# Kernel optimization log

Hardware: AMD Instinct MI355X
Metric: run time of the kernel (lower is better)

## Reference

```python
import jax, jax.numpy as jnp
import numpy as np

N, D_IM, D_CLI = 2048, 1024, 64
EPS = 1e-12  # F.normalize eps


def setup_inputs() -> dict:
    key = jax.random.key(0)
    k1, k2, k3, k4 = jax.random.split(key, 4)
    phi_im = jax.random.normal(k1, (N, D_IM), dtype=jnp.float32)
    phi_cli = jax.random.normal(k2, (N, D_CLI), dtype=jnp.float32)
    t = jax.random.randint(k3, (N, 2), 0, 3, dtype=jnp.int64)
    traumatic = jax.random.randint(k4, (N,), 0, 2, dtype=jnp.int64)
    return {"phi_im": phi_im, "phi_cli": phi_cli, "t": t, "traumatic": traumatic}


def _l2norm(x):
    n = jnp.sqrt(jnp.sum(x * x, axis=1, keepdims=True))
    return x / jnp.maximum(n, EPS)


def _pair_block(S, ma, mb):
    # S: [N,N] full cosine similarity; ma, mb: [N] bool group masks.
    valid = ma[:, None] & mb[None, :]
    mat = jnp.where(valid, S, 0.0)            # scatter-into-zero matrix semantics
    masked = jnp.where(valid, S, jnp.inf)     # masked argmin = nearest (least similar) pair
    flat = jnp.argmin(masked.reshape(-1))
    i = flat // S.shape[1]
    j = flat % S.shape[1]
    return mat, masked.reshape(-1)[flat], jnp.stack([i, j])


def reference(phi_im, phi_cli, t, traumatic):
    im_n = _l2norm(phi_im)
    cli_n = _l2norm(phi_cli)
    # single batched GEMM replaces the per-pair python loops
    S_im = im_n @ im_n.T    # [N,N]
    S_cli = cli_n @ cli_n.T  # [N,N]

    t1 = t[:, 1]
    m0 = (t1 == 0) & (traumatic == 1)
    m1 = t1 == 1
    m2 = t1 == 2

    mats, vals, idxs = [], [], []
    for S in (S_im, S_cli):
        for (ma, mb) in ((m0, m1), (m0, m2), (m1, m2)):
            mat, v, ij = _pair_block(S, ma, mb)
            mats.append(mat)
            vals.append(v)
            idxs.append(ij)
    sims = jnp.stack(mats)           # [6, N, N]: im_01, im_02, im_12, cli_01, cli_02, cli_12
    min_vals = jnp.stack(vals)       # [6]
    min_idx = jnp.stack(idxs)        # [6, 2]
    return sims, min_vals, min_idx
```

## Files before the change

### kernel.cpp

```cpp
#include <hip/hip_runtime.h>
#include <stdint.h>

#define NROW 2048
#define D_IM 1024
#define D_CLI 64
#define EPSF 1e-12f
#define NN ((size_t)NROW * (size_t)NROW)
#define GRID_GEMM 800
#define PIM_STRIDE 4352

typedef __attribute__((ext_vector_type(8))) short bf16x8;
typedef __attribute__((ext_vector_type(4))) float f32x4;

#define OFF_PACKED   0
#define OFF_CNT      64
#define OFF_CAT      128
#define OFF_LISTS    8320
#define OFF_POS      32896
#define OFF_COLINFO  41216
#define OFF_INVIM    65792
#define OFF_INVCLI   73984
#define OFF_PIM      82176
#define OFF_PCLI     8995072
#define OFF_SC       9519360

__device__ __forceinline__ unsigned int enc_f32(float x) {
    unsigned int u = __float_as_uint(x);
    return (u & 0x80000000u) ? ~u : (u | 0x80000000u);
}
__device__ __forceinline__ unsigned short bf16rn(float x) {
    unsigned int u = __float_as_uint(x);
    return (unsigned short)((u + 0x7FFFu + ((u >> 16) & 1u)) >> 16);
}
__device__ __forceinline__ float bf16tof(unsigned short h) {
    return __uint_as_float(((unsigned int)h) << 16);
}

__global__ __launch_bounds__(256)
void prepscan_kernel(const float* __restrict__ phi_im,
                     const float* __restrict__ phi_cli,
                     const int* __restrict__ t,
                     const int* __restrict__ traumatic,
                     float* __restrict__ inv_im,
                     float* __restrict__ inv_cli,
                     char* __restrict__ pim,
                     char* __restrict__ pcli,
                     int* __restrict__ cnt,
                     int* __restrict__ catArr,
                     int* __restrict__ lists,
                     int* __restrict__ posIn,
                     unsigned int* __restrict__ colinfo,
                     unsigned long long* __restrict__ packed,
                     float* __restrict__ out) {
    __shared__ unsigned long long shmem[256];
    const int tid = threadIdx.x;

    if (blockIdx.x > NROW) {
        const int row = blockIdx.x - (NROW + 1);
        const int t1 = t[2 * row + 1];
        const int tr = traumatic[row];
        if (t1 == 0 && tr == 1) return;
        float* orow = out + (size_t)row * NROW;
        const f32x4 z4 = (f32x4){0.f, 0.f, 0.f, 0.f};
        __builtin_nontemporal_store(z4, (f32x4*)orow + tid);
        __builtin_nontemporal_store(z4, (f32x4*)orow + tid + 256);
        return;
    }

    if (blockIdx.x == NROW) {
        int cats[8];
        unsigned long long mycnt = 0;
        #pragma unroll
        for (int e = 0; e < 8; e++) {
            int r = tid * 8 + e;
            int t1 = t[2 * r + 1];
            int tr = traumatic[r];
            int c = (t1 == 1) ? 1 : ((t1 == 2) ? 2 : ((tr == 1) ? 0 : 3));
            cats[e] = c;
            catArr[r] = c;
            if (c < 3) mycnt += 1ULL << (21 * c);
        }
        shmem[tid] = mycnt;
        __syncthreads();
        for (int off = 1; off < 256; off <<= 1) {
            unsigned long long v = (tid >= off) ? shmem[tid - off] : 0ULL;
            __syncthreads();
            shmem[tid] += v;
            __syncthreads();
        }
        unsigned long long excl = shmem[tid] - mycnt;
        unsigned long long tot = shmem[255];
        unsigned int loc[3];
        #pragma unroll
        for (int c = 0; c < 3; c++)
            loc[c] = (unsigned int)(excl >> (21 * c)) & 0x1FFFFFu;
        #pragma unroll
        for (int e = 0; e < 8; e++) {
            int r = tid * 8 + e;
            int c = cats[e];
            unsigned int slot = 0xFFFFFFFFu;
            if (c < 3) {
                slot = loc[c]++;
                lists[c * 2048 + slot] = r;
                posIn[r] = (int)slot;
            }
            colinfo[0 * 2048 + r] = (c == 1) ? slot : 0xFFFFFFFFu;
            colinfo[1 * 2048 + r] = (c == 2) ? slot : 0xFFFFFFFFu;
            colinfo[2 * 2048 + r] = (c == 2) ? slot : 0xFFFFFFFFu;
        }
        if (tid == 0) {
            cnt[0] = (int)(tot & 0x1FFFFFu);
            cnt[1] = (int)((tot >> 21) & 0x1FFFFFu);
            cnt[2] = (int)((tot >> 42) & 0x1FFFFFu);
            cnt[3] = 0;
        }
        if (tid < 6) packed[tid] = 0xFFFFFFFFFFFFFFFFULL;
        return;
    }

    float* sred = (float*)shmem;
    const int r = blockIdx.x;

    float4 v = ((const float4*)(phi_im + (size_t)r * D_IM))[tid];
    float a[4] = {v.x, v.y, v.z, v.w};
    unsigned short h4[4], l4[4];
    #pragma unroll
    for (int e = 0; e < 4; e++) {
        h4[e] = bf16rn(a[e]);
        l4[e] = bf16rn(a[e] - bf16tof(h4[e]));
    }
    {
        char* rowb = pim + (size_t)r * PIM_STRIDE + (tid >> 1) * 32 + (tid & 1) * 8;
        *(ushort4*)rowb = make_ushort4(h4[0], h4[1], h4[2], h4[3]);
        *(ushort4*)(rowb + 16) = make_ushort4(l4[0], l4[1], l4[2], l4[3]);
    }
    sred[tid] = a[0] * a[0] + a[1] * a[1] + a[2] * a[2] + a[3] * a[3];
    __syncthreads();
    for (int off = 128; off > 0; off >>= 1) {
        if (tid < off) sred[tid] += sred[tid + off];
        __syncthreads();
    }
    if (tid == 0) inv_im[r] = 1.0f / fmaxf(sqrtf(sred[0]), EPSF);

    if (tid < 16) {
        float4 c = ((const float4*)(phi_cli + (size_t)r * D_CLI))[tid];
        float b[4] = {c.x, c.y, c.z, c.w};
        unsigned short ch[4], cl[4];
        #pragma unroll
        for (int e = 0; e < 4; e++) {
            ch[e] = bf16rn(b[e]);
            cl[e] = bf16rn(b[e] - bf16tof(ch[e]));
        }
        char* rowb = pcli + (size_t)r * 256 + (tid >> 1) * 32 + (tid & 1) * 8;
        *(ushort4*)rowb = make_ushort4(ch[0], ch[1], ch[2], ch[3]);
        *(ushort4*)(rowb + 16) = make_ushort4(cl[0], cl[1], cl[2], cl[3]);
    }
    if (tid < 64) {
        float c = phi_cli[(size_t)r * D_CLI + tid];
        float cs = c * c;
        #pragma unroll
        for (int off = 32; off > 0; off >>= 1) cs += __shfl_down(cs, off, 64);
        if (tid == 0) inv_cli[r] = 1.0f / fmaxf(sqrtf(cs), EPSF);
    }
}

#define MFMA_SET(AH, AL, BH, BL)                                           \
    _Pragma("unroll") for (int lm = 0; lm < 2; lm++)                       \
        _Pragma("unroll") for (int ln = 0; ln < 2; ln++) {                 \
            acc[lm][ln] = __builtin_amdgcn_mfma_f32_16x16x32_bf16(         \
                AH[lm], BH[ln], acc[lm][ln], 0, 0, 0);                     \
            acc[lm][ln] = __builtin_amdgcn_mfma_f32_16x16x32_bf16(         \
                AH[lm], BL[ln], acc[lm][ln], 0, 0, 0);                     \
            acc[lm][ln] = __builtin_amdgcn_mfma_f32_16x16x32_bf16(         \
                AL[lm], BH[ln], acc[lm][ln], 0, 0, 0);                     \
        }

#define LOAD_REGS(RA, RB, OFF)                                             \
    RA[0] = *(const f32x4*)(pX + gA0 + (OFF));                             \
    RA[1] = *(const f32x4*)(pX + gA1 + (OFF));                             \
    RB[0] = *(const f32x4*)(pX + gB0 + (OFF));                             \
    RB[1] = *(const f32x4*)(pX + gB1 + (OFF));

#define STAGE_WRITE(B, RA, RB)                                             \
    *(f32x4*)(&sT[B][0][my_e][my_r * 16]) = RA[0];                         \
    *(f32x4*)(&sT[B][0][my_e][(32 + my_r) * 16]) = RA[1];                  \
    *(f32x4*)(&sT[B][1][my_e][my_r * 16]) = RB[0];                         \
    *(f32x4*)(&sT[B][1][my_e][(32 + my_r) * 16]) = RB[1];

#define COMPUTE(B)                                                         \
    {                                                                      \
        bf16x8 AH[2], AL[2], BH[2], BL[2];                                 \
        _Pragma("unroll") for (int q = 0; q < 2; q++) {                    \
            AH[q] = *(const bf16x8*)(&sT[B][0][2 * quad][aoff[q]]);        \
            AL[q] = *(const bf16x8*)(&sT[B][0][2 * quad + 1][aoff[q]]);    \
            BH[q] = *(const bf16x8*)(&sT[B][1][2 * quad][boff[q]]);        \
            BL[q] = *(const bf16x8*)(&sT[B][1][2 * quad + 1][boff[q]]);    \
        }                                                                  \
        MFMA_SET(AH, AL, BH, BL)                                           \
    }

__global__ __launch_bounds__(256, 2)
void gemm_kernel(const char* __restrict__ pim,
                 const char* __restrict__ pcli,
                 const float* __restrict__ inv_im,
                 const float* __restrict__ inv_cli,
                 const int* __restrict__ cnt,
                 const int* __restrict__ lists,
                 const int* __restrict__ catArr,
                 unsigned short* __restrict__ Sc,
                 float* __restrict__ out,
                 unsigned long long* __restrict__ packed) {
    const int tid = threadIdx.x;

    if (blockIdx.x >= GRID_GEMM) {
        const int b = blockIdx.x - GRID_GEMM;
        const int pzf = 1 + (b >> 11);
        const int row = b & 2047;
        const int p = (pzf < 3) ? pzf : pzf - 3;
        const int rowcat = (p == 2) ? 1 : 0;
        if (catArr[row] == rowcat) return;
        float* orow = out + (size_t)pzf * NN + (size_t)row * NROW;
        const f32x4 z4 = (f32x4){0.f, 0.f, 0.f, 0.f};
        __builtin_nontemporal_store(z4, (f32x4*)orow + tid);
        __builtin_nontemporal_store(z4, (f32x4*)orow + tid + 256);
        return;
    }

    __shared__ float sIA[64], sIB[64];
    __shared__ int sRA[64], sRB[64];
    __shared__ __align__(16) char sT[2][2][8][1040];

    const int n0 = cnt[0], n1 = cnt[1], n2 = cnt[2];
    const int tA = (n0 + 63) >> 6, tB = (n1 + 63) >> 6, tC = (n2 + 63) >> 6;
    const int T0 = tA * tB, T1 = tA * tC, T2 = tB * tC;
    const int tot = T0 + T1 + T2;
    int bid = blockIdx.x;
    if (bid >= 2 * tot) return;
    int z = 0;
    if (bid >= tot) { z = 1; bid -= tot; }
    const size_t s0 = (size_t)(tA << 6) * (tB << 6);
    const size_t s1 = (size_t)(tA << 6) * (tC << 6);
    const size_t s2 = (size_t)(tB << 6) * (tC << 6);
    size_t scoff = z ? (s0 + s1 + s2) : 0;
    int gx, nA, nB, nBpad, pp;
    const int *lA, *lB;
    if (bid < T0)           { pp = 0; gx = tB; nA = n0; nB = n1; lA = lists;        lB = lists + 2048; nBpad = tB << 6; }
    else if (bid < T0 + T1) { bid -= T0;      scoff += s0;      pp = 1; gx = tC; nA = n0; nB = n2; lA = lists;        lB = lists + 4096; nBpad = tC << 6; }
    else                    { bid -= T0 + T1; scoff += s0 + s1; pp = 2; gx = tC; nA = n1; nB = n2; lA = lists + 2048; lB = lists + 4096; nBpad = tC << 6; }
    const int by = bid / gx, bx = bid % gx;
    const int i0 = by << 6, j0 = bx << 6;
    const int pz = z * 3 + pp;

    const char* __restrict__ pX = z ? pcli : pim;
    const float* __restrict__ inv = z ? inv_cli : inv_im;
    const int nst = z ? (D_CLI / 32) : (D_IM / 32);
    const size_t stride = z ? 256 : PIM_STRIDE;
    const int lane = tid & 63;
    const int wid = tid >> 6;
    const int wr = wid >> 1;
    const int wc = wid & 1;

    if (tid < 64) {
        int ia = lA[min(i0 + tid, nA - 1)];
        int ib = lB[min(j0 + tid, nB - 1)];
        sRA[tid] = ia; sRB[tid] = ib;
        sIA[tid] = inv[ia]; sIB[tid] = inv[ib];
    }
    __syncthreads();

    const int mrow = lane & 15;
    const int quad = lane >> 4;

    const int my_e = tid & 7;
    const int my_r = tid >> 3;
    const size_t gA0 = (size_t)sRA[my_r] * stride + my_e * 16;
    const size_t gA1 = (size_t)sRA[32 + my_r] * stride + my_e * 16;
    const size_t gB0 = (size_t)sRB[my_r] * stride + my_e * 16;
    const size_t gB1 = (size_t)sRB[32 + my_r] * stride + my_e * 16;

    int aoff[2], boff[2];
    #pragma unroll
    for (int q = 0; q < 2; q++) {
        aoff[q] = ((wr * 2 + q) * 16 + mrow) * 16;
        boff[q] = ((wc * 2 + q) * 16 + mrow) * 16;
    }

    f32x4 acc[2][2];
    #pragma unroll
    for (int lm = 0; lm < 2; lm++)
        #pragma unroll
        for (int ln = 0; ln < 2; ln++)
            acc[lm][ln] = (f32x4){0.f, 0.f, 0.f, 0.f};

    f32x4 ra0[2], rb0[2], ra1[2], rb1[2];
    LOAD_REGS(ra0, rb0, 0);
    LOAD_REGS(ra1, rb1, 128);

    for (int st = 0; st < nst; st += 2) {
        STAGE_WRITE(0, ra0, rb0);
        __syncthreads();
        if (st + 2 < nst) { LOAD_REGS(ra0, rb0, (size_t)(st + 2) * 128); }
        COMPUTE(0);
        __syncthreads();

        STAGE_WRITE(1, ra1, rb1);
        __syncthreads();
        if (st + 3 < nst) { LOAD_REGS(ra1, rb1, (size_t)(st + 3) * 128); }
        COMPUTE(1);
        __syncthreads();
    }

    unsigned long long best = 0xFFFFFFFFFFFFFFFFULL;
    #pragma unroll
    for (int lm = 0; lm < 2; lm++)
        #pragma unroll
        for (int ln = 0; ln < 2; ln++) {
            const int cloc = (wc * 2 + ln) * 16 + mrow;
            const float ivb = sIB[cloc];
            const unsigned int jcol = (unsigned int)sRB[cloc];
            #pragma unroll
            for (int rr = 0; rr < 4; rr++) {
                const int rloc = (wr * 2 + lm) * 16 + quad * 4 + rr;
                float sv = acc[lm][ln][rr] * (sIA[rloc] * ivb);
                Sc[scoff + (size_t)(i0 + rloc) * nBpad + (j0 + cloc)] = bf16rn(sv);
                unsigned long long pk =
                    ((unsigned long long)enc_f32(sv) << 32) |
                    ((unsigned int)sRA[rloc] * (unsigned int)NROW + jcol);
                if (pk < best) best = pk;
            }
        }
    #pragma unroll
    for (int off = 32; off > 0; off >>= 1) {
        unsigned long long o = __shfl_down(best, off, 64);
        if (o < best) best = o;
    }
    if (lane == 0) atomicMin(&packed[pz], best);
}

__global__ __launch_bounds__(256)
void writer_kernel(const unsigned short* __restrict__ Sc,
                   const int* __restrict__ cnt,
                   const int* __restrict__ catArr,
                   const int* __restrict__ posIn,
                   const unsigned int* __restrict__ colinfo,
                   float* __restrict__ out,
                   const unsigned long long* __restrict__ packed) {
    const int b = blockIdx.x;
    const int tid = threadIdx.x;
    if (b == 6 * NROW) {
        const int p = tid;
        if (p < 6) {
            unsigned long long pk = packed[p];
            float v;
            unsigned int flat;
            if (pk == 0xFFFFFFFFFFFFFFFFULL) { v = __builtin_huge_valf(); flat = 0u; }
            else {
                unsigned int key = (unsigned int)(pk >> 32);
                flat = (unsigned int)pk;
                unsigned int bits = (key & 0x80000000u) ? (key ^ 0x80000000u) : ~key;
                v = __uint_as_float(bits);
            }
            out[6 * NN + p] = v;
            out[6 * NN + 6 + 2 * p + 0] = (float)(flat >> 11);
            out[6 * NN + 6 + 2 * p + 1] = (float)(flat & 2047u);
        }
        return;
    }
    const int pz = b >> 11;
    const int row = b & 2047;
    const int z = pz / 3, p = pz - 3 * z;

    const int rowcat = (p == 2) ? 1 : 0;
    if (catArr[row] != rowcat) {
        if (pz < 4) return;
        float* orow = out + (size_t)pz * NN + (size_t)row * NROW;
        const f32x4 z4 = (f32x4){0.f, 0.f, 0.f, 0.f};
        __builtin_nontemporal_store(z4, (f32x4*)orow + tid);
        __builtin_nontemporal_store(z4, (f32x4*)orow + tid + 256);
        return;
    }

    float* orow = out + (size_t)pz * NN + (size_t)row * NROW;

    const int n0 = cnt[0], n1 = cnt[1], n2 = cnt[2];
    const int tA = (n0 + 63) >> 6, tB = (n1 + 63) >> 6, tC = (n2 + 63) >> 6;
    const size_t s0 = (size_t)(tA << 6) * (tB << 6);
    const size_t s1 = (size_t)(tA << 6) * (tC << 6);
    const size_t s2 = (size_t)(tB << 6) * (tC << 6);
    size_t scoff = z ? (s0 + s1 + s2) : 0;
    int nBpad;
    if (p == 0)      { nBpad = tB << 6; }
    else if (p == 1) { scoff += s0;      nBpad = tC << 6; }
    else             { scoff += s0 + s1; nBpad = tC << 6; }

    const unsigned short* srow = Sc + scoff + (size_t)posIn[row] * nBpad;
    const uint4* cinfo4 = (const uint4*)(colinfo + p * 2048);

    #pragma unroll
    for (int seg = 0; seg < 2; seg++) {
        const int j4 = tid + seg * 256;
        uint4 inf = cinfo4[j4];
        f32x4 vv;
        vv[0] = (inf.x != 0xFFFFFFFFu) ? bf16tof(srow[inf.x]) : 0.f;
        vv[1] = (inf.y != 0xFFFFFFFFu) ? bf16tof(srow[inf.y]) : 0.f;
        vv[2] = (inf.z != 0xFFFFFFFFu) ? bf16tof(srow[inf.z]) : 0.f;
        vv[3] = (inf.w != 0xFFFFFFFFu) ? bf16tof(srow[inf.w]) : 0.f;
        __builtin_nontemporal_store(vv, (f32x4*)orow + j4);
    }
}

extern "C" void kernel_launch(void* const* d_in, const int* in_sizes, int n_in,
                              void* d_out, int out_size, void* d_ws, size_t ws_size,
                              hipStream_t stream) {
    const float* phi_im = (const float*)d_in[0];
    const float* phi_cli = (const float*)d_in[1];
    const int* t = (const int*)d_in[2];
    const int* traumatic = (const int*)d_in[3];
    float* out = (float*)d_out;

    char* ws = (char*)d_ws;
    unsigned long long* packed = (unsigned long long*)(ws + OFF_PACKED);
    int* cnt = (int*)(ws + OFF_CNT);
    int* catArr = (int*)(ws + OFF_CAT);
    int* lists = (int*)(ws + OFF_LISTS);
    int* posIn = (int*)(ws + OFF_POS);
    unsigned int* colinfo = (unsigned int*)(ws + OFF_COLINFO);
    float* inv_im = (float*)(ws + OFF_INVIM);
    float* inv_cli = (float*)(ws + OFF_INVCLI);
    char* pim = ws + OFF_PIM;
    char* pcli = ws + OFF_PCLI;
    unsigned short* Sc = (unsigned short*)(ws + OFF_SC);

    prepscan_kernel<<<2 * NROW + 1, 256, 0, stream>>>(
        phi_im, phi_cli, t, traumatic, inv_im, inv_cli, pim, pcli,
        cnt, catArr, lists, posIn, colinfo, packed, out);
    gemm_kernel<<<GRID_GEMM + 3 * NROW, 256, 0, stream>>>(
        pim, pcli, inv_im, inv_cli, cnt, lists, catArr, Sc, out, packed);
    writer_kernel<<<6 * NROW + 1, 256, 0, stream>>>(Sc, cnt, catArr, posIn,
                                                    colinfo, out, packed);
}
```

Baseline: 168.0 us.

## Move all output zero-fill into GEMM kernel; writer iterates compacted row lists

Zero-filling of the six output matrices moves out of the prep kernel and the writer into the GEMM kernel's tail blocks. Those blocks now clear every row unconditionally, two rows per block. The writer indexes rows through the compacted per-group lists, so it only launches useful work for valid rows and no longer needs the category or position lookups. The clinical norm is folded into the existing bf16 split loop, and the GEMM launch bound is raised to 3 blocks per CU. The cost is that valid rows are written twice (zeros, then values), which adds HBM traffic, and the higher occupancy target may limit GEMM registers.

```diff
diff --git a/kernel.cpp b/kernel.cpp
--- a/kernel.cpp
+++ b/kernel.cpp
@@ -50,22 +50,9 @@
                      int* __restrict__ lists,
                      int* __restrict__ posIn,
                      unsigned int* __restrict__ colinfo,
-                     unsigned long long* __restrict__ packed,
-                     float* __restrict__ out) {
+                     unsigned long long* __restrict__ packed) {
     __shared__ unsigned long long shmem[256];
     const int tid = threadIdx.x;
-
-    if (blockIdx.x > NROW) {
-        const int row = blockIdx.x - (NROW + 1);
-        const int t1 = t[2 * row + 1];
-        const int tr = traumatic[row];
-        if (t1 == 0 && tr == 1) return;
-        float* orow = out + (size_t)row * NROW;
-        const f32x4 z4 = (f32x4){0.f, 0.f, 0.f, 0.f};
-        __builtin_nontemporal_store(z4, (f32x4*)orow + tid);
-        __builtin_nontemporal_store(z4, (f32x4*)orow + tid + 256);
-        return;
-    }
 
     if (blockIdx.x == NROW) {
         int cats[8];
@@ -154,12 +141,9 @@
         char* rowb = pcli + (size_t)r * 256 + (tid >> 1) * 32 + (tid & 1) * 8;
         *(ushort4*)rowb = make_ushort4(ch[0], ch[1], ch[2], ch[3]);
         *(ushort4*)(rowb + 16) = make_ushort4(cl[0], cl[1], cl[2], cl[3]);
-    }
-    if (tid < 64) {
-        float c = phi_cli[(size_t)r * D_CLI + tid];
-        float cs = c * c;
-        #pragma unroll
-        for (int off = 32; off > 0; off >>= 1) cs += __shfl_down(cs, off, 64);
+        float cs = b[0] * b[0] + b[1] * b[1] + b[2] * b[2] + b[3] * b[3];
+        #pragma unroll
+        for (int off = 8; off > 0; off >>= 1) cs += __shfl_down(cs, off, 16);
         if (tid == 0) inv_cli[r] = 1.0f / fmaxf(sqrtf(cs), EPSF);
     }
 }
@@ -199,30 +183,27 @@
         MFMA_SET(AH, AL, BH, BL)                                           \
     }
 
-__global__ __launch_bounds__(256, 2)
+__global__ __launch_bounds__(256, 3)
 void gemm_kernel(const char* __restrict__ pim,
                  const char* __restrict__ pcli,
                  const float* __restrict__ inv_im,
                  const float* __restrict__ inv_cli,
                  const int* __restrict__ cnt,
                  const int* __restrict__ lists,
-                 const int* __restrict__ catArr,
                  unsigned short* __restrict__ Sc,
                  float* __restrict__ out,
                  unsigned long long* __restrict__ packed) {
     const int tid = threadIdx.x;
 
     if (blockIdx.x >= GRID_GEMM) {
-        const int b = blockIdx.x - GRID_GEMM;
-        const int pzf = 1 + (b >> 11);
-        const int row = b & 2047;
-        const int p = (pzf < 3) ? pzf : pzf - 3;
-        const int rowcat = (p == 2) ? 1 : 0;
-        if (catArr[row] == rowcat) return;
-        float* orow = out + (size_t)pzf * NN + (size_t)row * NROW;
+        const int idx = blockIdx.x - GRID_GEMM;
+        const int pzf = idx >> 10;
+        const int rp = idx & 1023;
+        float* orow = out + (size_t)pzf * NN + (size_t)(2 * rp) * NROW;
         const f32x4 z4 = (f32x4){0.f, 0.f, 0.f, 0.f};
-        __builtin_nontemporal_store(z4, (f32x4*)orow + tid);
-        __builtin_nontemporal_store(z4, (f32x4*)orow + tid + 256);
+        #pragma unroll
+        for (int s = 0; s < 4; s++)
+            __builtin_nontemporal_store(z4, (f32x4*)orow + tid + s * 256);
         return;
     }
 
@@ -340,8 +321,7 @@
 __global__ __launch_bounds__(256)
 void writer_kernel(const unsigned short* __restrict__ Sc,
                    const int* __restrict__ cnt,
-                   const int* __restrict__ catArr,
-                   const int* __restrict__ posIn,
+                   const int* __restrict__ lists,
                    const unsigned int* __restrict__ colinfo,
                    float* __restrict__ out,
                    const unsigned long long* __restrict__ packed) {
@@ -367,22 +347,16 @@
         return;
     }
     const int pz = b >> 11;
-    const int row = b & 2047;
+    const int k = b & 2047;
     const int z = pz / 3, p = pz - 3 * z;
 
-    const int rowcat = (p == 2) ? 1 : 0;
-    if (catArr[row] != rowcat) {
-        if (pz < 4) return;
-        float* orow = out + (size_t)pz * NN + (size_t)row * NROW;
-        const f32x4 z4 = (f32x4){0.f, 0.f, 0.f, 0.f};
-        __builtin_nontemporal_store(z4, (f32x4*)orow + tid);
-        __builtin_nontemporal_store(z4, (f32x4*)orow + tid + 256);
-        return;
-    }
+    const int n0 = cnt[0], n1 = cnt[1], n2 = cnt[2];
+    const int nv = (p == 2) ? n1 : n0;
+    if (k >= nv) return;
+    const int row = lists[((p == 2) ? 1 : 0) * 2048 + k];
 
     float* orow = out + (size_t)pz * NN + (size_t)row * NROW;
 
-    const int n0 = cnt[0], n1 = cnt[1], n2 = cnt[2];
     const int tA = (n0 + 63) >> 6, tB = (n1 + 63) >> 6, tC = (n2 + 63) >> 6;
     const size_t s0 = (size_t)(tA << 6) * (tB << 6);
     const size_t s1 = (size_t)(tA << 6) * (tC << 6);
@@ -393,7 +367,7 @@
     else if (p == 1) { scoff += s0;      nBpad = tC << 6; }
     else             { scoff += s0 + s1; nBpad = tC << 6; }
 
-    const unsigned short* srow = Sc + scoff + (size_t)posIn[row] * nBpad;
+    const unsigned short* srow = Sc + scoff + (size_t)k * nBpad;
     const uint4* cinfo4 = (const uint4*)(colinfo + p * 2048);
 
     #pragma unroll
@@ -431,11 +405,11 @@
     char* pcli = ws + OFF_PCLI;
     unsigned short* Sc = (unsigned short*)(ws + OFF_SC);
 
-    prepscan_kernel<<<2 * NROW + 1, 256, 0, stream>>>(
+    prepscan_kernel<<<NROW + 1, 256, 0, stream>>>(
         phi_im, phi_cli, t, traumatic, inv_im, inv_cli, pim, pcli,
-        cnt, catArr, lists, posIn, colinfo, packed, out);
-    gemm_kernel<<<GRID_GEMM + 3 * NROW, 256, 0, stream>>>(
-        pim, pcli, inv_im, inv_cli, cnt, lists, catArr, Sc, out, packed);
-    writer_kernel<<<6 * NROW + 1, 256, 0, stream>>>(Sc, cnt, catArr, posIn,
+        cnt, catArr, lists, posIn, colinfo, packed);
+    gemm_kernel<<<GRID_GEMM + 6 * 1024, 256, 0, stream>>>(
+        pim, pcli, inv_im, inv_cli, cnt, lists, Sc, out, packed);
+    writer_kernel<<<6 * NROW + 1, 256, 0, stream>>>(Sc, cnt, lists,
                                                     colinfo, out, packed);
 }
```

New measurement: 169.2 us. Within noise of the previous version (+0.7%).
